# Optimization experiments

Measured on AMD Instinct MI355X. Metric: run time of the kernel, lower is better.

## Reference

```python
import jax, jax.numpy as jnp
import numpy as np

N_NODES = 100000
N_EDGES = 625000
F_IN = 128
N_CLASS = 32
K_HOPS = 2


def setup_inputs() -> dict:
    key = jax.random.key(0)
    k1, k2, k3 = jax.random.split(key, 3)
    x = jax.random.normal(k1, (N_NODES, F_IN), dtype=jnp.float32)
    edge_index = jax.random.randint(k2, (2, N_EDGES), 0, N_NODES, dtype=jnp.int64)
    # Linear(features_num, num_class) params (Kaiming-uniform-ish scale)
    lim = 1.0 / np.sqrt(F_IN)
    W = jax.random.uniform(k3, (N_CLASS, F_IN), dtype=jnp.float32, minval=-lim, maxval=lim)
    b = jnp.zeros((N_CLASS,), dtype=jnp.float32)
    return {"x": x, "edge_index": edge_index, "W": W, "b": b}


def reference(x, edge_index, W, b):
    n = x.shape[0]
    # gcn_norm with added self-loops (edge_weight = 1)
    loop = jnp.arange(n, dtype=edge_index.dtype)
    src = jnp.concatenate([edge_index[0], loop])  # j (source)
    dst = jnp.concatenate([edge_index[1], loop])  # i (target)
    ones = jnp.ones(src.shape[0], dtype=x.dtype)
    deg = jax.ops.segment_sum(ones, dst, num_segments=n)
    dinv = jnp.where(deg > 0, jax.lax.rsqrt(deg), 0.0)
    norm = dinv[src] * dinv[dst]  # [E+N]

    # K hops of propagation: out[i] = sum_j norm_ij * x[j]
    for _ in range(K_HOPS):
        x = jax.ops.segment_sum(norm[:, None] * x[src], dst, num_segments=n)

    logits = x @ W.T + b  # [N, num_class]
    return jax.nn.log_softmax(logits, axis=-1)
```

## Files before the change

kernel.cpp:

```cpp
#include <hip/hip_runtime.h>
#include <hip/hip_bf16.h>

constexpr int NN = 100000;
constexpr int NE = 625000;
constexpr int F  = 128;
constexpr int C  = 32;
constexpr int CH  = F / 4;
constexpr int CQ  = C / 4;
constexpr int NB  = (NN + 255) / 256;

__global__ void k_zero(int* __restrict__ cnt) {
    int i = blockIdx.x * blockDim.x + threadIdx.x;
    if (i < NN) cnt[i] = 0;
}

__global__ void k_count(const int* __restrict__ dstA, int* __restrict__ cnt) {
    int e = blockIdx.x * blockDim.x + threadIdx.x;
    if (e < NE) atomicAdd(&cnt[dstA[e]], 1);
}

__global__ void k_dinv(const int* __restrict__ cnt, float* __restrict__ dinv) {
    int i = blockIdx.x * blockDim.x + threadIdx.x;
    if (i < NN) dinv[i] = rsqrtf((float)(cnt[i] + 1));
}

__global__ __launch_bounds__(256) void k_blocksum(const int* __restrict__ cnt,
                                                  int* __restrict__ blocksums) {
    int idx = blockIdx.x * 256 + threadIdx.x;
    int v = (idx < NN) ? cnt[idx] : 0;
    #pragma unroll
    for (int off = 32; off; off >>= 1) v += __shfl_down(v, off, 64);
    __shared__ int ws[4];
    int lane = threadIdx.x & 63, wid = threadIdx.x >> 6;
    if (lane == 0) ws[wid] = v;
    __syncthreads();
    if (threadIdx.x == 0)
        blocksums[blockIdx.x] = ws[0] + ws[1] + ws[2] + ws[3];
}

__global__ __launch_bounds__(512) void k_scanB(const int* __restrict__ blocksums,
                                               int* __restrict__ blockoff,
                                               int* __restrict__ rowptr) {
    __shared__ int s[512];
    int t = threadIdx.x;
    s[t] = (t < NB) ? blocksums[t] : 0;
    __syncthreads();
    for (int off = 1; off < 512; off <<= 1) {
        int v = (t >= off) ? s[t - off] : 0;
        __syncthreads();
        s[t] += v;
        __syncthreads();
    }
    if (t < NB) blockoff[t] = (t == 0) ? 0 : s[t - 1];
    if (t == NB - 1) rowptr[NN] = s[t];
}

__global__ __launch_bounds__(256) void k_scanC(const int* __restrict__ cnt,
                                               const int* __restrict__ blockoff,
                                               int* __restrict__ rowptr,
                                               int* __restrict__ cursor) {
    __shared__ int s[256];
    int t = threadIdx.x;
    int idx = blockIdx.x * 256 + t;
    int val = (idx < NN) ? cnt[idx] : 0;
    s[t] = val;
    __syncthreads();
    for (int off = 1; off < 256; off <<= 1) {
        int v = (t >= off) ? s[t - off] : 0;
        __syncthreads();
        s[t] += v;
        __syncthreads();
    }
    if (idx < NN) {
        int r = blockoff[blockIdx.x] + s[t] - val;
        rowptr[idx] = r;
        cursor[idx] = r;
    }
}

__global__ void k_fill(const int* __restrict__ srcA, const int* __restrict__ dstA,
                       const float* __restrict__ dinv, int* __restrict__ cursor,
                       int* __restrict__ col, float* __restrict__ wgt) {
    int e = blockIdx.x * blockDim.x + threadIdx.x;
    if (e >= NE) return;
    int s = srcA[e], d = dstA[e];
    int pos = atomicAdd(&cursor[d], 1);
    col[pos] = s;
    wgt[pos] = dinv[s] * dinv[d];
}

__global__ __launch_bounds__(256) void k_proj(const float* __restrict__ x,
                                              const float* __restrict__ W,
                                              float* __restrict__ z) {
    __shared__ float Ws[C * F];
    for (int i = threadIdx.x; i < C * F; i += 256) Ws[i] = W[i];
    __syncthreads();

    int node = blockIdx.x * blockDim.x + threadIdx.x;
    if (node >= NN) return;

    float acc[C];
    #pragma unroll
    for (int c = 0; c < C; ++c) acc[c] = 0.f;

    const float4* xr = (const float4*)(x + (long)node * F);
    #pragma unroll 4
    for (int q = 0; q < CH; ++q) {
        float4 xv = xr[q];
        #pragma unroll
        for (int c = 0; c < C; ++c) {
            float4 wv = ((const float4*)Ws)[c * CH + q];
            acc[c] += xv.x * wv.x + xv.y * wv.y + xv.z * wv.z + xv.w * wv.w;
        }
    }
    float4* zp = (float4*)(z + (long)node * C);
    #pragma unroll
    for (int q = 0; q < CQ; ++q)
        zp[q] = make_float4(acc[q*4+0], acc[q*4+1], acc[q*4+2], acc[q*4+3]);
}

__global__ void k_gather(const float* __restrict__ zin, const int* __restrict__ rowptr,
                         const int* __restrict__ col, const float* __restrict__ wgt,
                         const float* __restrict__ dinv, float* __restrict__ zout) {
    int t = blockIdx.x * blockDim.x + threadIdx.x;
    if (t >= NN * CQ) return;
    int node = t >> 3;
    int q    = t & 7;
    float dn = dinv[node];
    float4 v = ((const float4*)zin)[node * CQ + q];
    float c  = dn * dn;
    float ax = c * v.x, ay = c * v.y, az = c * v.z, aw = c * v.w;
    int e0 = rowptr[node], e1 = rowptr[node + 1];
    for (int e = e0; e < e1; ++e) {
        int   s = col[e];
        float w = wgt[e];
        float4 u = ((const float4*)zin)[s * CQ + q];
        ax += w * u.x; ay += w * u.y; az += w * u.z; aw += w * u.w;
    }
    ((float4*)zout)[node * CQ + q] = make_float4(ax, ay, az, aw);
}

__global__ void k_finish(const float* __restrict__ z, const float* __restrict__ b,
                         float* __restrict__ out) {
    int node = blockIdx.x * blockDim.x + threadIdx.x;
    if (node >= NN) return;
    float v[C];
    const float4* zp = (const float4*)(z + (long)node * C);
    #pragma unroll
    for (int q = 0; q < CQ; ++q) {
        float4 t = zp[q];
        v[q*4+0] = t.x + b[q*4+0];
        v[q*4+1] = t.y + b[q*4+1];
        v[q*4+2] = t.z + b[q*4+2];
        v[q*4+3] = t.w + b[q*4+3];
    }
    float m = v[0];
    #pragma unroll
    for (int c = 1; c < C; ++c) m = fmaxf(m, v[c]);
    float s = 0.f;
    #pragma unroll
    for (int c = 0; c < C; ++c) s += expf(v[c] - m);
    float lse = m + logf(s);
    float4* op = (float4*)(out + (long)node * C);
    #pragma unroll
    for (int q = 0; q < CQ; ++q)
        op[q] = make_float4(v[q*4+0]-lse, v[q*4+1]-lse, v[q*4+2]-lse, v[q*4+3]-lse);
}

extern "C" void kernel_launch(void* const* d_in, const int* in_sizes, int n_in,
                              void* d_out, int out_size, void* d_ws, size_t ws_size,
                              hipStream_t stream) {
    const float* x  = (const float*)d_in[0];
    const int*   ei = (const int*)d_in[1];
    const float* W  = (const float*)d_in[2];
    const float* b  = (const float*)d_in[3];
    float* out = (float*)d_out;

    const int* srcA = ei;
    const int* dstA = ei + NE;

    char* p = (char*)d_ws;
    auto alloc = [&](size_t bytes) { char* r = p; p += (bytes + 255) & ~(size_t)255; return r; };
    int*   cnt       = (int*)  alloc(sizeof(int) * NN);
    float* dinv      = (float*)alloc(sizeof(float) * NN);
    int*   rowptr    = (int*)  alloc(sizeof(int) * (NN + 1));
    int*   cursor    = (int*)  alloc(sizeof(int) * NN);
    int*   blocksums = (int*)  alloc(sizeof(int) * NB);
    int*   blockoff  = (int*)  alloc(sizeof(int) * NB);
    int*   col       = (int*)  alloc(sizeof(int) * NE);
    float* wgt       = (float*)alloc(sizeof(float) * NE);
    float* z0        = (float*)alloc(sizeof(float) * (size_t)NN * C);
    float* z1        = (float*)alloc(sizeof(float) * (size_t)NN * C);
    float* z2        = z0;

    k_zero    <<<(NN + 255) / 256, 256, 0, stream>>>(cnt);
    k_count   <<<(NE + 255) / 256, 256, 0, stream>>>(dstA, cnt);
    k_dinv    <<<(NN + 255) / 256, 256, 0, stream>>>(cnt, dinv);
    k_blocksum<<<NB, 256, 0, stream>>>(cnt, blocksums);
    k_scanB   <<<1, 512, 0, stream>>>(blocksums, blockoff, rowptr);
    k_scanC   <<<NB, 256, 0, stream>>>(cnt, blockoff, rowptr, cursor);
    k_fill    <<<(NE + 255) / 256, 256, 0, stream>>>(srcA, dstA, dinv, cursor, col, wgt);

    k_proj<<<(NN + 255) / 256, 256, 0, stream>>>(x, W, z0);

    int gthreads = NN * CQ;
    k_gather<<<(gthreads + 255) / 256, 256, 0, stream>>>(z0, rowptr, col, wgt, dinv, z1);
    k_gather<<<(gthreads + 255) / 256, 256, 0, stream>>>(z1, rowptr, col, wgt, dinv, z2);

    k_finish<<<(NN + 255) / 256, 256, 0, stream>>>(z2, b, out);
}
```

Baseline: 171.6 us.

## Split projection across four threads per node and fuse hop two with log-softmax

The projection kernel now gives each node four threads, each computing eight output classes and reading W straight from global/cache instead of staging it in shared memory. This raises parallelism and cuts per-thread register use. The second propagation hop is fused with bias add and log-softmax, with the row max and sum reduced across four lanes by shuffles, which removes one launch and one full round trip of the intermediate. The trade-off is that each thread in the fused kernel does wider 32-byte gathers per edge, and the projection reads x four times, once per thread.

```diff
diff --git a/kernel.cpp b/kernel.cpp
--- a/kernel.cpp
+++ b/kernel.cpp
@@ -5,7 +5,6 @@
 constexpr int NE = 625000;
 constexpr int F  = 128;
 constexpr int C  = 32;
-constexpr int CH  = F / 4;
 constexpr int CQ  = C / 4;
 constexpr int NB  = (NN + 255) / 256;
 
@@ -92,31 +91,30 @@
 __global__ __launch_bounds__(256) void k_proj(const float* __restrict__ x,
                                               const float* __restrict__ W,
                                               float* __restrict__ z) {
-    __shared__ float Ws[C * F];
-    for (int i = threadIdx.x; i < C * F; i += 256) Ws[i] = W[i];
-    __syncthreads();
-
-    int node = blockIdx.x * blockDim.x + threadIdx.x;
-    if (node >= NN) return;
-
-    float acc[C];
-    #pragma unroll
-    for (int c = 0; c < C; ++c) acc[c] = 0.f;
-
-    const float4* xr = (const float4*)(x + (long)node * F);
+    int t = blockIdx.x * 256 + threadIdx.x;
+    if (t >= NN * 4) return;
+    int node = t >> 2;
+    int qr   = t & 3;
+
+    const float4* xr = (const float4*)(x + (size_t)node * F);
+    const float4* Wr = (const float4*)(W + (size_t)qr * 8 * F);
+
+    float acc[8];
+    #pragma unroll
+    for (int c = 0; c < 8; ++c) acc[c] = 0.f;
+
     #pragma unroll 4
-    for (int q = 0; q < CH; ++q) {
+    for (int q = 0; q < F / 4; ++q) {
         float4 xv = xr[q];
         #pragma unroll
-        for (int c = 0; c < C; ++c) {
-            float4 wv = ((const float4*)Ws)[c * CH + q];
+        for (int c = 0; c < 8; ++c) {
+            float4 wv = Wr[c * (F / 4) + q];
             acc[c] += xv.x * wv.x + xv.y * wv.y + xv.z * wv.z + xv.w * wv.w;
         }
     }
-    float4* zp = (float4*)(z + (long)node * C);
-    #pragma unroll
-    for (int q = 0; q < CQ; ++q)
-        zp[q] = make_float4(acc[q*4+0], acc[q*4+1], acc[q*4+2], acc[q*4+3]);
+    float4* zp = (float4*)(z + (size_t)node * C + qr * 8);
+    zp[0] = make_float4(acc[0], acc[1], acc[2], acc[3]);
+    zp[1] = make_float4(acc[4], acc[5], acc[6], acc[7]);
 }
 
 __global__ void k_gather(const float* __restrict__ zin, const int* __restrict__ rowptr,
@@ -140,31 +138,55 @@
     ((float4*)zout)[node * CQ + q] = make_float4(ax, ay, az, aw);
 }
 
-__global__ void k_finish(const float* __restrict__ z, const float* __restrict__ b,
-                         float* __restrict__ out) {
-    int node = blockIdx.x * blockDim.x + threadIdx.x;
-    if (node >= NN) return;
-    float v[C];
-    const float4* zp = (const float4*)(z + (long)node * C);
-    #pragma unroll
-    for (int q = 0; q < CQ; ++q) {
-        float4 t = zp[q];
-        v[q*4+0] = t.x + b[q*4+0];
-        v[q*4+1] = t.y + b[q*4+1];
-        v[q*4+2] = t.z + b[q*4+2];
-        v[q*4+3] = t.w + b[q*4+3];
-    }
+__global__ __launch_bounds__(256) void k_hop2_finish(const float* __restrict__ zin,
+                                                     const int* __restrict__ rowptr,
+                                                     const int* __restrict__ col,
+                                                     const float* __restrict__ wgt,
+                                                     const float* __restrict__ dinv,
+                                                     const float* __restrict__ b,
+                                                     float* __restrict__ out) {
+    int t = blockIdx.x * 256 + threadIdx.x;
+    if (t >= NN * 4) return;
+    int node = t >> 2;
+    int qr   = t & 3;
+
+    float dn = dinv[node];
+    float cc = dn * dn;
+    const float4* zrow = (const float4*)(zin + (size_t)node * C) + qr * 2;
+    float4 a0 = zrow[0], a1 = zrow[1];
+    a0.x *= cc; a0.y *= cc; a0.z *= cc; a0.w *= cc;
+    a1.x *= cc; a1.y *= cc; a1.z *= cc; a1.w *= cc;
+
+    int e0 = rowptr[node], e1 = rowptr[node + 1];
+    for (int e = e0; e < e1; ++e) {
+        int   s = col[e];
+        float w = wgt[e];
+        const float4* u = (const float4*)(zin + (size_t)s * C) + qr * 2;
+        float4 u0 = u[0], u1 = u[1];
+        a0.x += w * u0.x; a0.y += w * u0.y; a0.z += w * u0.z; a0.w += w * u0.w;
+        a1.x += w * u1.x; a1.y += w * u1.y; a1.z += w * u1.z; a1.w += w * u1.w;
+    }
+
+    float4 b0 = ((const float4*)b)[qr * 2];
+    float4 b1 = ((const float4*)b)[qr * 2 + 1];
+    float v[8] = { a0.x + b0.x, a0.y + b0.y, a0.z + b0.z, a0.w + b0.w,
+                   a1.x + b1.x, a1.y + b1.y, a1.z + b1.z, a1.w + b1.w };
+
     float m = v[0];
     #pragma unroll
-    for (int c = 1; c < C; ++c) m = fmaxf(m, v[c]);
+    for (int c = 1; c < 8; ++c) m = fmaxf(m, v[c]);
+    m = fmaxf(m, __shfl_xor(m, 1, 64));
+    m = fmaxf(m, __shfl_xor(m, 2, 64));
     float s = 0.f;
     #pragma unroll
-    for (int c = 0; c < C; ++c) s += expf(v[c] - m);
+    for (int c = 0; c < 8; ++c) s += expf(v[c] - m);
+    s += __shfl_xor(s, 1, 64);
+    s += __shfl_xor(s, 2, 64);
     float lse = m + logf(s);
-    float4* op = (float4*)(out + (long)node * C);
-    #pragma unroll
-    for (int q = 0; q < CQ; ++q)
-        op[q] = make_float4(v[q*4+0]-lse, v[q*4+1]-lse, v[q*4+2]-lse, v[q*4+3]-lse);
+
+    float4* op = (float4*)(out + (size_t)node * C + qr * 8);
+    op[0] = make_float4(v[0]-lse, v[1]-lse, v[2]-lse, v[3]-lse);
+    op[1] = make_float4(v[4]-lse, v[5]-lse, v[6]-lse, v[7]-lse);
 }
 
 extern "C" void kernel_launch(void* const* d_in, const int* in_sizes, int n_in,
@@ -191,7 +213,6 @@
     float* wgt       = (float*)alloc(sizeof(float) * NE);
     float* z0        = (float*)alloc(sizeof(float) * (size_t)NN * C);
     float* z1        = (float*)alloc(sizeof(float) * (size_t)NN * C);
-    float* z2        = z0;
 
     k_zero    <<<(NN + 255) / 256, 256, 0, stream>>>(cnt);
     k_count   <<<(NE + 255) / 256, 256, 0, stream>>>(dstA, cnt);
@@ -201,11 +222,8 @@
     k_scanC   <<<NB, 256, 0, stream>>>(cnt, blockoff, rowptr, cursor);
     k_fill    <<<(NE + 255) / 256, 256, 0, stream>>>(srcA, dstA, dinv, cursor, col, wgt);
 
-    k_proj<<<(NN + 255) / 256, 256, 0, stream>>>(x, W, z0);
-
-    int gthreads = NN * CQ;
-    k_gather<<<(gthreads + 255) / 256, 256, 0, stream>>>(z0, rowptr, col, wgt, dinv, z1);
-    k_gather<<<(gthreads + 255) / 256, 256, 0, stream>>>(z1, rowptr, col, wgt, dinv, z2);
-
-    k_finish<<<(NN + 255) / 256, 256, 0, stream>>>(z2, b, out);
-}
+    k_proj<<<(NN * 4 + 255) / 256, 256, 0, stream>>>(x, W, z0);
+
+    k_gather<<<(NN * CQ + 255) / 256, 256, 0, stream>>>(z0, rowptr, col, wgt, dinv, z1);
+    k_hop2_finish<<<(NN * 4 + 255) / 256, 256, 0, stream>>>(z1, rowptr, col, wgt, dinv, b, out);
+}
```

Result: slower. 320.0 us (+86.5%).
